# Kernel optimization log

Measured on AMD Instinct MI355X. Metric: run time of the kernel, lower is better.

The kernel has to match this reference:

```python
import jax, jax.numpy as jnp
import numpy as np

B, S, H = 8, 4096, 1024
AVG_WORD_LEN = 4
NUM_SEGMENTS = (B * S) // AVG_WORD_LEN  # 8192 words total


def setup_inputs() -> dict:
    key = jax.random.key(0)
    hidden_states = jax.random.normal(key, (B, S, H), dtype=jnp.float32)
    # Contiguous word spans of length AVG_WORD_LEN covering every token,
    # encoded as a per-token segment id over the flattened (B*S) axis.
    segment_ids = jnp.arange(B * S, dtype=jnp.int64) // AVG_WORD_LEN
    return {
        "hidden_states": hidden_states,
        "segment_ids": segment_ids,
        "num_segments": NUM_SEGMENTS,
    }


def reference(hidden_states, segment_ids, num_segments):
    # hidden_states: [B, S, H]; segment_ids: [B*S] mapping token -> word index.
    b, s, h = hidden_states.shape
    flat = hidden_states.reshape(b * s, h)                      # [B*S, H]
    sums = jax.ops.segment_sum(flat, segment_ids, num_segments=num_segments)  # [W, H]
    counts = jax.ops.segment_sum(
        jnp.ones((b * s,), dtype=hidden_states.dtype), segment_ids,
        num_segments=num_segments,
    )                                                           # [W]
    # pooling_type == 'average': mean over each word span (empty spans -> 0,
    # matching torch which skips zero-length words).
    return sums / jnp.maximum(counts, 1.0)[:, None]
```

## Files before the change

### kernel.cpp

```cpp
#include <hip/hip_runtime.h>

#define H_DIM 1024
#define H4 (H_DIM / 4)

typedef float f32x4 __attribute__((ext_vector_type(4)));

__global__ void WordPooling_fused_kernel(const float* __restrict__ x,
                                         const int* __restrict__ seg,
                                         int n_tokens,
                                         float* __restrict__ out) {
    int w = blockIdx.x;
    int h = threadIdx.x;

    int lo = 0, hi = n_tokens;
    while (lo < hi) {
        int mid = (lo + hi) >> 1;
        if (seg[mid] < w) lo = mid + 1; else hi = mid;
    }
    int st = lo;
    int cnt = 0;
    while (st + cnt < n_tokens && seg[st + cnt] == w) ++cnt;

    const f32x4* p = (const f32x4*)x + (size_t)st * H4 + h;
    f32x4 acc = (f32x4)(0.0f);
    if (cnt == 4) {
        f32x4 v0 = __builtin_nontemporal_load(p);
        f32x4 v1 = __builtin_nontemporal_load(p + H4);
        f32x4 v2 = __builtin_nontemporal_load(p + 2 * H4);
        f32x4 v3 = __builtin_nontemporal_load(p + 3 * H4);
        acc = ((v0 + v1) + v2) + v3;
        acc *= 0.25f;
    } else {
        for (int i = 0; i < cnt; ++i)
            acc += __builtin_nontemporal_load(p + (size_t)i * H4);
        acc *= 1.0f / fmaxf((float)cnt, 1.0f);
    }
    __builtin_nontemporal_store(acc, (f32x4*)out + (size_t)w * H4 + h);
}

extern "C" void kernel_launch(void* const* d_in, const int* in_sizes, int n_in,
                              void* d_out, int out_size, void* d_ws, size_t ws_size,
                              hipStream_t stream) {
    const float* x  = (const float*)d_in[0];
    const int* seg  = (const int*)d_in[1];
    int n_tokens    = in_sizes[1];
    int W           = out_size / H_DIM;

    WordPooling_fused_kernel<<<W, H4, 0, stream>>>(x, seg, n_tokens, (float*)d_out);
}
```

Before: 31.40 us.

## Process eight words per block with guessed-start galloping search and wave ballot counts

Each block now handles eight consecutive words instead of one. It finds the first token with a galloping search seeded by a proportional guess rather than a full binary search, then derives the per-word counts from one 64-token window load using ballot/popcount. This cuts the per-word segment-id search overhead and the number of blocks, but it leaves fewer blocks (1024) to hide memory latency and runs the word loop serially within each block.

```diff
diff --git a/kernel.cpp b/kernel.cpp
--- a/kernel.cpp
+++ b/kernel.cpp
@@ -2,40 +2,78 @@
 
 #define H_DIM 1024
 #define H4 (H_DIM / 4)
+#define WPB 8
 
 typedef float f32x4 __attribute__((ext_vector_type(4)));
 
-__global__ void WordPooling_fused_kernel(const float* __restrict__ x,
-                                         const int* __restrict__ seg,
-                                         int n_tokens,
-                                         float* __restrict__ out) {
-    int w = blockIdx.x;
+__global__ void __launch_bounds__(256)
+WordPooling_fused_kernel(const float* __restrict__ x,
+                         const int* __restrict__ seg,
+                         int n_tokens, int W,
+                         float* __restrict__ out) {
+    int w0 = blockIdx.x * WPB;
     int h = threadIdx.x;
+    int lane = threadIdx.x & 63;
 
-    int lo = 0, hi = n_tokens;
-    while (lo < hi) {
-        int mid = (lo + hi) >> 1;
-        if (seg[mid] < w) lo = mid + 1; else hi = mid;
+    int st = 0;
+    if (w0 > 0) {
+        int g = (int)((long long)w0 * n_tokens / W);
+        if (g > n_tokens - 1) g = n_tokens - 1;
+        int lo, hi;
+        if (seg[g] >= w0) {
+            int step = 1;
+            while (step <= g && seg[g - step] >= w0) step <<= 1;
+            lo = (step <= g) ? g - step : -1;
+            hi = g - (step >> 1);
+        } else {
+            int step = 1;
+            while (g + step < n_tokens && seg[g + step] < w0) step <<= 1;
+            lo = g + (step >> 1);
+            hi = (g + step < n_tokens) ? g + step : n_tokens;
+        }
+        while (hi - lo > 1) {
+            int mid = (lo + hi) >> 1;
+            if (seg[mid] < w0) lo = mid; else hi = mid;
+        }
+        st = hi;
     }
-    int st = lo;
-    int cnt = 0;
-    while (st + cnt < n_tokens && seg[st + cnt] == w) ++cnt;
 
-    const f32x4* p = (const f32x4*)x + (size_t)st * H4 + h;
-    f32x4 acc = (f32x4)(0.0f);
-    if (cnt == 4) {
-        f32x4 v0 = __builtin_nontemporal_load(p);
-        f32x4 v1 = __builtin_nontemporal_load(p + H4);
-        f32x4 v2 = __builtin_nontemporal_load(p + 2 * H4);
-        f32x4 v3 = __builtin_nontemporal_load(p + 3 * H4);
-        acc = ((v0 + v1) + v2) + v3;
-        acc *= 0.25f;
-    } else {
-        for (int i = 0; i < cnt; ++i)
-            acc += __builtin_nontemporal_load(p + (size_t)i * H4);
-        acc *= 1.0f / fmaxf((float)cnt, 1.0f);
+    int wlast = w0 + WPB - 1;
+    if (wlast > W - 1) wlast = W - 1;
+
+    int idx = st + lane;
+    int sv = (idx < n_tokens) ? seg[idx] : 0x7FFFFFFF;
+    bool windowed = (__ballot(sv > wlast) != 0ULL);
+
+    const f32x4* x4 = (const f32x4*)x;
+    f32x4* out4 = (f32x4*)out;
+
+    int cur = st;
+    for (int w = w0; w <= wlast; ++w) {
+        int cnt;
+        if (windowed) {
+            cnt = (int)__popcll(__ballot(sv == w));
+        } else {
+            cnt = 0;
+            while (cur + cnt < n_tokens && seg[cur + cnt] == w) ++cnt;
+        }
+        const f32x4* p = x4 + (size_t)cur * H4 + h;
+        f32x4 acc;
+        if (cnt == 4) {
+            f32x4 v0 = __builtin_nontemporal_load(p);
+            f32x4 v1 = __builtin_nontemporal_load(p + H4);
+            f32x4 v2 = __builtin_nontemporal_load(p + 2 * H4);
+            f32x4 v3 = __builtin_nontemporal_load(p + 3 * H4);
+            acc = (((v0 + v1) + v2) + v3) * 0.25f;
+        } else {
+            acc = (f32x4)(0.0f);
+            for (int i = 0; i < cnt; ++i)
+                acc += __builtin_nontemporal_load(p + (size_t)i * H4);
+            acc *= 1.0f / fmaxf((float)cnt, 1.0f);
+        }
+        __builtin_nontemporal_store(acc, out4 + (size_t)w * H4 + h);
+        cur += cnt;
     }
-    __builtin_nontemporal_store(acc, (f32x4*)out + (size_t)w * H4 + h);
 }
 
 extern "C" void kernel_launch(void* const* d_in, const int* in_sizes, int n_in,
@@ -46,5 +84,6 @@
     int n_tokens    = in_sizes[1];
     int W           = out_size / H_DIM;
 
-    WordPooling_fused_kernel<<<W, H4, 0, stream>>>(x, seg, n_tokens, (float*)d_out);
+    int grid = (W + WPB - 1) / WPB;
+    WordPooling_fused_kernel<<<grid, H4, 0, stream>>>(x, seg, n_tokens, W, (float*)d_out);
 }
```

After: 31.51 us. No clear change (+0.3%).
